# Optimization experiments

Measured on AMD Instinct MI355X. Metric: run time of the kernel, lower is better.

## Reference

```python
import jax, jax.numpy as jnp
import numpy as np

N = 100000
E = 1600000
F_IN = 128
HDIM = 64
HEADS = 8
C1 = HDIM // HEADS  # 8 per-head channels in conv1
NUM_CLASSES = 2
NUM_GRAPHS = 64
NEG_SLOPE = 0.2


def setup_inputs() -> dict:
    key = jax.random.key(0)
    ks = jax.random.split(key, 12)
    x = jax.random.normal(ks[0], (N, F_IN), dtype=jnp.float32)
    edge_index = jax.random.randint(ks[1], (2, E), 0, N, dtype=jnp.int64)
    batch = jnp.sort(jax.random.randint(ks[2], (N,), 0, NUM_GRAPHS, dtype=jnp.int64))
    # conv1 params (Glorot-ish scale)
    W1 = jax.random.normal(ks[3], (F_IN, HEADS * C1), dtype=jnp.float32) * (1.0 / np.sqrt(F_IN))
    att_src1 = jax.random.normal(ks[4], (HEADS, C1), dtype=jnp.float32) * 0.1
    att_dst1 = jax.random.normal(ks[5], (HEADS, C1), dtype=jnp.float32) * 0.1
    b1 = jnp.zeros((HEADS * C1,), dtype=jnp.float32)
    # conv2 params (1 head, no concat)
    W2 = jax.random.normal(ks[6], (HDIM, 1 * NUM_CLASSES), dtype=jnp.float32) * (1.0 / np.sqrt(HDIM))
    att_src2 = jax.random.normal(ks[7], (1, NUM_CLASSES), dtype=jnp.float32) * 0.1
    att_dst2 = jax.random.normal(ks[8], (1, NUM_CLASSES), dtype=jnp.float32) * 0.1
    b2 = jnp.zeros((NUM_CLASSES,), dtype=jnp.float32)
    return {"x": x, "edge_index": edge_index, "batch": batch,
            "W1": W1, "att_src1": att_src1, "att_dst1": att_dst1, "b1": b1,
            "W2": W2, "att_src2": att_src2, "att_dst2": att_dst2, "b2": b2}


def gat_conv(x, src, dst, W, a_src, a_dst, b, heads, ch, concat):
    # PyG GATConv: linear proj -> per-edge attention -> segment softmax over dst -> scatter-add
    n = x.shape[0]
    h = (x @ W).reshape(n, heads, ch)                      # [N,H,C]
    alpha_s = jnp.einsum('nhc,hc->nh', h, a_src)           # [N,H]
    alpha_d = jnp.einsum('nhc,hc->nh', h, a_dst)           # [N,H]
    e = jax.nn.leaky_relu(alpha_s[src] + alpha_d[dst], NEG_SLOPE)  # [E,H]
    m = jax.ops.segment_max(e, dst, num_segments=n)        # stable softmax per dst
    e = jnp.exp(e - m[dst])
    denom = jax.ops.segment_sum(e, dst, num_segments=n) + 1e-16
    alpha = e / denom[dst]                                 # [E,H]
    msg = h[src] * alpha[:, :, None]                       # [E,H,C]
    out = jax.ops.segment_sum(msg, dst, num_segments=n)    # [N,H,C]
    if concat:
        out = out.reshape(n, heads * ch)
    else:
        out = out.mean(axis=1)
    return out + b


def reference(x, edge_index, batch, W1, att_src1, att_dst1, b1, W2, att_src2, att_dst2, b2):
    # PyG GATConv default add_self_loops=True
    loops = jnp.arange(N, dtype=edge_index.dtype)
    src = jnp.concatenate([edge_index[0], loops])
    dst = jnp.concatenate([edge_index[1], loops])
    h = gat_conv(x, src, dst, W1, att_src1, att_dst1, b1, HEADS, C1, concat=True)
    h = jax.nn.relu(h)
    # F.dropout with training=False (eval mode) -> identity
    h = gat_conv(h, src, dst, W2, att_src2, att_dst2, b2, 1, NUM_CLASSES, concat=False)
    # global_mean_pool over batch ids
    sums = jax.ops.segment_sum(h, batch, num_segments=NUM_GRAPHS)
    cnts = jax.ops.segment_sum(jnp.ones((N,), h.dtype), batch, num_segments=NUM_GRAPHS)
    pooled = sums / jnp.maximum(cnts, 1.0)[:, None]        # [G, num_classes]
    return jax.nn.log_softmax(pooled, axis=1)
```

## Files before the change

kernel.cpp:

```cpp
#include <hip/hip_runtime.h>
#include <hip/hip_bf16.h>
#include <hip/hip_fp16.h>
#include <math.h>

#define NN 100000
#define EE 1600000
#define ET 1700000
#define NEG_SLOPE 0.2f
#define XS_STRIDE 136
#define L2E 1.44269504088896f

#define BKB 8
#define BKSZ 256
#define NBUCK 391
#define SLAB 8192
#define PAD 32
#define EPT2 16
#define CHUNK2 (256 * EPT2)
#define NCH2 ((ET + CHUNK2 - 1) / CHUNK2)

typedef _Float16 f16;
typedef f16 f16x8 __attribute__((ext_vector_type(8)));
typedef float f32x4 __attribute__((ext_vector_type(4)));
typedef float f32x2 __attribute__((ext_vector_type(2)));

__device__ __forceinline__ float leaky(float v) {
    return fmaxf(v, NEG_SLOPE * v);
}
__device__ __forceinline__ unsigned char enc_fp8(float v) {
    int pk = __builtin_amdgcn_cvt_pk_fp8_f32(v, 0.f, 0, false);
    return (unsigned char)(pk & 0xff);
}

__device__ __forceinline__ void fold8(float (&dst)[8], const float (&X)[8],
                                      const float (&Y)[8], int sb, int off) {
#pragma unroll
    for (int i = 0; i < 8; ++i) {
        float m = sb ? Y[i] : X[i];
        float o = sb ? X[i] : Y[i];
        dst[i] = m + __shfl_xor(o, off, 64);
    }
}


__global__ __launch_bounds__(256) void convert_w_kernel(
        const float* __restrict__ W1, f16* __restrict__ wt,
        unsigned char* __restrict__ nrec) {
    int i = blockIdx.x * 256 + threadIdx.x;
    if (i < 128 * 64) {
        int n = i >> 7, k = i & 127;
        wt[n * 128 + k] = (f16)W1[k * 64 + n];
    }
    if (blockIdx.x == 0 && threadIdx.x < 8) {
        uint4* dr = (uint4*)(nrec + (size_t)NN * 128);
        dr[threadIdx.x] = make_uint4(0u, 0u, 0xFC00u, 0u);
    }
}

__global__ __launch_bounds__(256) void gemm1_mfma(
        const float* __restrict__ x, const f16* __restrict__ wt,
        const float* __restrict__ att_s, const float* __restrict__ att_d,
        unsigned char* __restrict__ nrec) {
    __shared__ f16 xs[64 * XS_STRIDE];
    const int tid = threadIdx.x;
    const int node0 = blockIdx.x * 64;
    for (int i = tid; i < 64 * 64; i += 256) {
        int r = i >> 6, cp = i & 63;
        int n = node0 + r;
        float2 v = (n < NN) ? ((const float2*)x)[(long)n * 64 + cp]
                            : make_float2(0.f, 0.f);
        xs[r * XS_STRIDE + 2 * cp]     = (f16)v.x;
        xs[r * XS_STRIDE + 2 * cp + 1] = (f16)v.y;
    }
    __syncthreads();
    const int wv = tid >> 6;
    const int lane = tid & 63;
    const int n16 = lane & 15;
    const int quad = lane >> 4;
    f16x8 bf[4][4];
#pragma unroll
    for (int t = 0; t < 4; ++t)
#pragma unroll
        for (int kk = 0; kk < 4; ++kk)
            bf[t][kk] = *(const f16x8*)(wt + ((t * 16 + n16) * 128 + kk * 32 + quad * 8));
    f32x4 acc[4] = {{0,0,0,0},{0,0,0,0},{0,0,0,0},{0,0,0,0}};
#pragma unroll
    for (int kk = 0; kk < 4; ++kk) {
        f16x8 af = *(const f16x8*)(xs + ((wv * 16 + n16) * XS_STRIDE + kk * 32 + quad * 8));
#pragma unroll
        for (int t = 0; t < 4; ++t)
            acc[t] = __builtin_amdgcn_mfma_f32_16x16x32_f16(af, bf[t][kk], acc[t], 0, 0, 0);
    }
    float ats[4], atd[4];
#pragma unroll
    for (int t = 0; t < 4; ++t) {
        ats[t] = att_s[t * 16 + n16];
        atd[t] = att_d[t * 16 + n16];
    }
    const int head = (n16 >> 3);
    const int chpos = n16 & 7;
#pragma unroll
    for (int t = 0; t < 4; ++t)
#pragma unroll
        for (int r = 0; r < 4; ++r) {
            int m = node0 + wv * 16 + quad * 4 + r;
            bool ok = (m < NN);
            if (ok)
                nrec[(size_t)m * 128 + (t * 2 + head) * 16 + chpos] =
                    enc_fp8(acc[t][r]);
            float vs = acc[t][r] * ats[t];
            float vd = acc[t][r] * atd[t];
            vs += __shfl_xor(vs, 1, 64); vd += __shfl_xor(vd, 1, 64);
            vs += __shfl_xor(vs, 2, 64); vd += __shfl_xor(vd, 2, 64);
            vs += __shfl_xor(vs, 4, 64); vd += __shfl_xor(vd, 4, 64);
            if (ok && chpos == 0) {
                unsigned char* nb = nrec + (size_t)m * 128 + (t * 2 + head) * 16;
                *(__half*)(nb + 8)  = __float2half_rn(vs * L2E);
                *(float*)(nb + 12) = vd * L2E;
            }
        }
}

__global__ __launch_bounds__(256) void bucket_fill(
        const int* __restrict__ ei, int* __restrict__ bcur,
        unsigned* __restrict__ gpay) {
    __shared__ int lcnt[NBUCK];
    __shared__ int gbase[NBUCK];
    const int tid = threadIdx.x;
    for (int i = tid; i < NBUCK; i += 256) lcnt[i] = 0;
    __syncthreads();
    const int base = blockIdx.x * CHUNK2 + tid;
    unsigned pay[EPT2];
    int bk[EPT2], pos[EPT2];
#pragma unroll
    for (int k = 0; k < EPT2; ++k) {
        int e = base + k * 256;
        if (e < ET) {
            int s, d;
            if (e < EE) {
                s = __builtin_nontemporal_load(ei + e);
                d = __builtin_nontemporal_load(ei + EE + e);
            } else { s = d = e - EE; }
            int b = d >> BKB;
            bk[k] = b;
            pay[k] = ((unsigned)(d & (BKSZ - 1)) << 17) | (unsigned)s;
            pos[k] = atomicAdd(&lcnt[b], 1);
        } else bk[k] = -1;
    }
    __syncthreads();
    for (int i = tid; i < NBUCK; i += 256)
        gbase[i] = lcnt[i] ? (i * SLAB + atomicAdd(&bcur[i * PAD], lcnt[i])) : 0;
    __syncthreads();
#pragma unroll
    for (int k = 0; k < EPT2; ++k)
        if (bk[k] >= 0) gpay[gbase[bk[k]] + pos[k]] = pay[k];
}

__global__ __launch_bounds__(256) void fine_csr(
        const unsigned* __restrict__ gpay, const int* __restrict__ bcur,
        int* __restrict__ rowptr, int* __restrict__ rowend,
        int* __restrict__ csr_src) {
    __shared__ int cnt[BKSZ];
    __shared__ int ts[256];
    const int b = blockIdx.x;
    const int tid = threadIdx.x;
    const int off = b * SLAB;
    int blen = bcur[b * PAD];
    if (blen > SLAB) blen = SLAB;
    const int d0 = b << BKB;
    cnt[tid] = 0;
    __syncthreads();
    for (int i = tid; i < blen; i += 256)
        atomicAdd(&cnt[gpay[off + i] >> 17], 1);
    __syncthreads();
    int v = cnt[tid];
    int vp = (v + 7) & ~7;
    ts[tid] = vp;
    __syncthreads();
    for (int o = 1; o < 256; o <<= 1) {
        int u = (tid >= o) ? ts[tid - o] : 0;
        __syncthreads();
        ts[tid] += u;
        __syncthreads();
    }
    int excl = ts[tid] - vp;
    if (excl + vp > SLAB) vp = v;
    cnt[tid] = excl;
    int d = d0 + tid;
    if (d < NN) {
        rowptr[d] = off + excl;
        rowend[d] = off + excl + v;
    }
    for (int i = v; i < vp; ++i) csr_src[off + excl + i] = NN;
    __syncthreads();
    for (int i = tid; i < blen; i += 256) {
        unsigned pay = gpay[off + i];
        int pos = atomicAdd(&cnt[pay >> 17], 1);
        csr_src[off + pos] = (int)(pay & 0x1FFFFu);
    }
}

__global__ __launch_bounds__(256) void conv1_fused_kernel(
        const int* __restrict__ rowptr, const int* __restrict__ rowend,
        const int* __restrict__ csr_src, const unsigned char* __restrict__ nrec,
        const float* __restrict__ b1, const float* __restrict__ W2,
        const float* __restrict__ as2, const float* __restrict__ ad2,
        float4* __restrict__ rec) {
    const int tid = threadIdx.x;
    const int wv = tid >> 6;
    const int c = tid & 63;
    const int slot = c >> 3;
    const int hd = c & 7;
    const int sb0 = slot & 1, sb1 = (slot >> 1) & 1, sb2 = (slot >> 2) & 1;
    int n0 = __builtin_amdgcn_readfirstlane((blockIdx.x * 4 + wv) * 4);
    const float adA = *(const float*)(nrec + ((size_t)(n0 + 0) << 7) + (hd << 4) + 12);
    const float adB = *(const float*)(nrec + ((size_t)(n0 + 1) << 7) + (hd << 4) + 12);
    const float adC = *(const float*)(nrec + ((size_t)(n0 + 2) << 7) + (hd << 4) + 12);
    const float adD = *(const float*)(nrec + ((size_t)(n0 + 3) << 7) + (hd << 4) + 12);
    int jA = rowptr[n0 + 0], eA = jA + ((rowend[n0 + 0] - jA + 7) & ~7);
    int jB = rowptr[n0 + 1], eB = jB + ((rowend[n0 + 1] - jB + 7) & ~7);
    int jC = rowptr[n0 + 2], eC = jC + ((rowend[n0 + 2] - jC + 7) & ~7);
    int jD = rowptr[n0 + 3], eD = jD + ((rowend[n0 + 3] - jD + 7) & ~7);
    float accA[8] = {0,0,0,0,0,0,0,0}, accB[8] = {0,0,0,0,0,0,0,0};
    float accC[8] = {0,0,0,0,0,0,0,0}, accD[8] = {0,0,0,0,0,0,0,0};
    float lA = 0.f, lB = 0.f, lC = 0.f, lD = 0.f;

#define STEP(j, e, ad, l, acc)                                               \
    {                                                                        \
        int jj = (j) < (e) - 8 ? (j) : (e) - 8;        \
        int src = csr_src[jj + slot];                                        \
        uint4 v = *(const uint4*)(nrec + (((size_t)src << 7) | (hd << 4)));  \
        unsigned short ush = (unsigned short)v.z;                            \
        float as = __half2float(*(const __half*)&ush);                       \
        float p = exp2f(leaky(as + (ad)));                                   \
        p = ((j) < (e)) ? p : 0.f;                                           \
        f32x2 f01 = __builtin_amdgcn_cvt_pk_f32_fp8((int)v.x, 0);            \
        f32x2 f23 = __builtin_amdgcn_cvt_pk_f32_fp8((int)v.x, 1);            \
        f32x2 f45 = __builtin_amdgcn_cvt_pk_f32_fp8((int)v.y, 0);            \
        f32x2 f67 = __builtin_amdgcn_cvt_pk_f32_fp8((int)v.y, 1);            \
        (l) += p;                                                            \
        acc[0] += p * f01.x; acc[1] += p * f01.y;                            \
        acc[2] += p * f23.x; acc[3] += p * f23.y;                            \
        acc[4] += p * f45.x; acc[5] += p * f45.y;                            \
        acc[6] += p * f67.x; acc[7] += p * f67.y;                            \
        (j) += 8;                                                            \
    }

    while (jA < eA || jB < eB || jC < eC || jD < eD) {
        STEP(jA, eA, adA, lA, accA);
        STEP(jB, eB, adB, lB, accB);
        STEP(jC, eC, adC, lC, accC);
        STEP(jD, eD, adD, lD, accD);
    }
#undef STEP

    float P[8], Q[8];
    fold8(P, accA, accB, sb0, 8);
    fold8(Q, accC, accD, sb0, 8);
    float lP, lQ, lm, lo;
    lm = sb0 ? lB : lA; lo = sb0 ? lA : lB;
    lP = lm + __shfl_xor(lo, 8, 64);
    lm = sb0 ? lD : lC; lo = sb0 ? lC : lD;
    lQ = lm + __shfl_xor(lo, 8, 64);
    float R[8];
    fold8(R, P, Q, sb1, 16);
    lm = sb1 ? lQ : lP; lo = sb1 ? lP : lQ;
    float l = lm + __shfl_xor(lo, 16, 64);
    float S[4];
#pragma unroll
    for (int i = 0; i < 4; ++i) {
        float m = sb2 ? R[i + 4] : R[i];
        float o = sb2 ? R[i] : R[i + 4];
        S[i] = m + __shfl_xor(o, 32, 64);
    }
    l += __shfl_xor(l, 32, 64);
    const int cb = (hd << 3) + sb2 * 4;
    float inv = 1.f / (l + 1e-16f);
    float4 bb = *(const float4*)(b1 + cb);
    float4 w01 = *(const float4*)(W2 + cb * 2);
    float4 w23 = *(const float4*)(W2 + cb * 2 + 4);
    float v0 = fmaxf(S[0] * inv + bb.x, 0.f);
    float v1 = fmaxf(S[1] * inv + bb.y, 0.f);
    float v2 = fmaxf(S[2] * inv + bb.z, 0.f);
    float v3 = fmaxf(S[3] * inv + bb.w, 0.f);
    float r0 = v0 * w01.x + v1 * w01.z + v2 * w23.x + v3 * w23.z;
    float r1 = v0 * w01.y + v1 * w01.w + v2 * w23.y + v3 * w23.w;
    r0 += __shfl_xor(r0, 1, 64);  r1 += __shfl_xor(r1, 1, 64);
    r0 += __shfl_xor(r0, 2, 64);  r1 += __shfl_xor(r1, 2, 64);
    r0 += __shfl_xor(r0, 4, 64);  r1 += __shfl_xor(r1, 4, 64);
    r0 += __shfl_xor(r0, 32, 64); r1 += __shfl_xor(r1, 32, 64);
    if (hd == 0 && sb2 == 0) {
        int n = n0 + sb1 * 2 + sb0;
        rec[n] = make_float4((r0 * as2[0] + r1 * as2[1]) * L2E, r0, r1,
                             (r0 * ad2[0] + r1 * ad2[1]) * L2E);
    }
}

__global__ __launch_bounds__(256) void conv2_pool_kernel(
        const int* __restrict__ rowptr, const int* __restrict__ rowend,
        const int* __restrict__ csr_src, const float4* __restrict__ rec,
        const int* __restrict__ batch,
        float* __restrict__ pooled ) {
    __shared__ float ls[192];
    int tid = threadIdx.x;
    if (tid < 192) ls[tid] = 0.f;
    __syncthreads();
    int n = blockIdx.x * 256 + tid;
    if (n < NN) {
        float adn = rec[n].w;
        int jb = rowptr[n], je = rowend[n];
        float l0 = 0.f, l1 = 0.f, l2 = 0.f, l3 = 0.f;
        float x0 = 0.f, x1 = 0.f, x2 = 0.f, x3 = 0.f;
        float y0 = 0.f, y1 = 0.f, y2 = 0.f, y3 = 0.f;
        int j = jb;
        int i0 = csr_src[j], i1 = csr_src[j + 1];
        int i2 = csr_src[j + 2], i3 = csr_src[j + 3];
        for (; j + 3 < je; ) {
            float4 ra = rec[i0];
            float4 rb = rec[i1];
            float4 rc = rec[i2];
            float4 rd = rec[i3];
            j += 4;
            i0 = csr_src[j] & 0x1FFFF;     i1 = csr_src[j + 1] & 0x1FFFF;
            i2 = csr_src[j + 2] & 0x1FFFF; i3 = csr_src[j + 3] & 0x1FFFF;
            float pa = exp2f(leaky(ra.x + adn));
            float pb = exp2f(leaky(rb.x + adn));
            float pc = exp2f(leaky(rc.x + adn));
            float pd = exp2f(leaky(rd.x + adn));
            l0 += pa; x0 += pa * ra.y; y0 += pa * ra.z;
            l1 += pb; x1 += pb * rb.y; y1 += pb * rb.z;
            l2 += pc; x2 += pc * rc.y; y2 += pc * rc.z;
            l3 += pd; x3 += pd * rd.y; y3 += pd * rd.z;
        }
        for (; j < je; ++j) {
            float4 ra = rec[csr_src[j]];
            float pa = exp2f(leaky(ra.x + adn));
            l0 += pa; x0 += pa * ra.y; y0 += pa * ra.z;
        }
        float l = (l0 + l1) + (l2 + l3);
        float xx = (x0 + x1) + (x2 + x3);
        float yy = (y0 + y1) + (y2 + y3);
        float inv = 1.f / (l + 1e-16f);
        int g = batch[n];
        atomicAdd(&ls[g * 2],     xx * inv);
        atomicAdd(&ls[g * 2 + 1], yy * inv);
        atomicAdd(&ls[128 + g],   1.f);
    }
    __syncthreads();
    if (tid < 192) atomicAdd(&pooled[tid], ls[tid]);
}

__global__ __launch_bounds__(64) void final_kernel(
        const float* __restrict__ pooled, const float* __restrict__ b2,
        float* __restrict__ out) {
    int g = threadIdx.x;
    if (g >= 64) return;
    float c = pooled[128 + g];
    float denom = c > 1.f ? c : 1.f;
    float p0 = pooled[g * 2] / denom + b2[0];
    float p1 = pooled[g * 2 + 1] / denom + b2[1];
    float m = fmaxf(p0, p1);
    float lse = m + logf(expf(p0 - m) + expf(p1 - m));
    out[g * 2] = p0 - lse;
    out[g * 2 + 1] = p1 - lse;
}

extern "C" void kernel_launch(void* const* d_in, const int* in_sizes, int n_in,
                              void* d_out, int out_size, void* d_ws, size_t ws_size,
                              hipStream_t stream) {
    const float* x   = (const float*)d_in[0];
    const int*   ei  = (const int*)d_in[1];
    const int*   bat = (const int*)d_in[2];
    const float* W1  = (const float*)d_in[3];
    const float* as1 = (const float*)d_in[4];
    const float* ad1 = (const float*)d_in[5];
    const float* b1  = (const float*)d_in[6];
    const float* W2  = (const float*)d_in[7];
    const float* as2 = (const float*)d_in[8];
    const float* ad2 = (const float*)d_in[9];
    const float* b2  = (const float*)d_in[10];
    float* out = (float*)d_out;

    float* ws = (float*)d_ws;
    const long off_nrec   = 0;
    const long off_wt     = off_nrec + (long)(NN + 1) * 32;
    const long off_rec    = off_wt + 4096;
    const long off_rowptr = off_rec + (long)NN * 4;
    const long off_rowend = off_rowptr + NN;
    const long off_gpay   = off_rowend + NN;
    const long off_csr    = off_gpay + (long)NBUCK * SLAB;
    const long off_zero   = off_csr + (long)NBUCK * SLAB;
    const long off_bcur   = off_zero;
    const long off_pool   = off_bcur + NBUCK * PAD;
    const long zero_elems = off_pool + 192 - off_zero;

    hipMemsetAsync(ws + off_zero, 0, zero_elems * sizeof(float), stream);

    convert_w_kernel<<<32, 256, 0, stream>>>(W1, (f16*)(ws + off_wt),
                                             (unsigned char*)(ws + off_nrec));
    gemm1_mfma<<<(NN + 63) / 64, 256, 0, stream>>>(
        x, (const f16*)(ws + off_wt), as1, ad1,
        (unsigned char*)(ws + off_nrec));

    bucket_fill<<<NCH2, 256, 0, stream>>>(ei, (int*)(ws + off_bcur),
                                          (unsigned*)(ws + off_gpay));
    fine_csr<<<NBUCK, 256, 0, stream>>>(
        (const unsigned*)(ws + off_gpay), (const int*)(ws + off_bcur),
        (int*)(ws + off_rowptr), (int*)(ws + off_rowend),
        (int*)(ws + off_csr));

    conv1_fused_kernel<<<NN / 16, 256, 0, stream>>>(
        (const int*)(ws + off_rowptr), (const int*)(ws + off_rowend),
        (const int*)(ws + off_csr), (const unsigned char*)(ws + off_nrec),
        b1, W2, as2, ad2, (float4*)(ws + off_rec));

    conv2_pool_kernel<<<(NN + 255) / 256, 256, 0, stream>>>(
        (const int*)(ws + off_rowptr), (const int*)(ws + off_rowend),
        (const int*)(ws + off_csr), (const float4*)(ws + off_rec),
        bat, ws + off_pool);

    final_kernel<<<1, 64, 0, stream>>>(ws + off_pool, b2, out);
}
```

Before: 229.6 us.

## Fuse small kernels, halve bucket size, split conv2 rows over 4 lanes

Folds the weight conversion into bucket_fill and the final log-softmax into conv2_pool_kernel through a last-block-done counter, which removes two kernel launches. Bucket size drops from 256 to 128 nodes, doubling the number of fine_csr blocks. Each conv2 node is now handled by four lanes combined with shuffles, and the x load in gemm1 is widened to float4. Risks include the extra atomic and fence at the end of conv2, and slab overflow with the smaller 4096 slab.

```diff
diff --git a/kernel.cpp b/kernel.cpp
--- a/kernel.cpp
+++ b/kernel.cpp
@@ -10,16 +10,17 @@
 #define XS_STRIDE 136
 #define L2E 1.44269504088896f
 
-#define BKB 8
-#define BKSZ 256
-#define NBUCK 391
-#define SLAB 8192
+#define BKB 7
+#define BKSZ 128
+#define NBUCK 782
+#define SLAB 4096
 #define PAD 32
 #define EPT2 16
 #define CHUNK2 (256 * EPT2)
 #define NCH2 ((ET + CHUNK2 - 1) / CHUNK2)
 
 typedef _Float16 f16;
+typedef f16 f16x4 __attribute__((ext_vector_type(4)));
 typedef f16 f16x8 __attribute__((ext_vector_type(8)));
 typedef float f32x4 __attribute__((ext_vector_type(4)));
 typedef float f32x2 __attribute__((ext_vector_type(2)));
@@ -43,18 +44,49 @@
 }
 
 
-__global__ __launch_bounds__(256) void convert_w_kernel(
-        const float* __restrict__ W1, f16* __restrict__ wt,
-        unsigned char* __restrict__ nrec) {
-    int i = blockIdx.x * 256 + threadIdx.x;
-    if (i < 128 * 64) {
+__global__ __launch_bounds__(256) void bucket_fill(
+        const int* __restrict__ ei, int* __restrict__ bcur,
+        unsigned* __restrict__ gpay, const float* __restrict__ W1,
+        f16* __restrict__ wt, unsigned char* __restrict__ nrec) {
+    const int tid = threadIdx.x;
+    if (blockIdx.x < 32) {
+        int i = blockIdx.x * 256 + tid;
         int n = i >> 7, k = i & 127;
         wt[n * 128 + k] = (f16)W1[k * 64 + n];
     }
-    if (blockIdx.x == 0 && threadIdx.x < 8) {
+    if (blockIdx.x == 32 && tid < 8) {
         uint4* dr = (uint4*)(nrec + (size_t)NN * 128);
-        dr[threadIdx.x] = make_uint4(0u, 0u, 0xFC00u, 0u);
-    }
+        dr[tid] = make_uint4(0u, 0u, 0xFC00u, 0u);
+    }
+    __shared__ int lcnt[NBUCK];
+    __shared__ int gbase[NBUCK];
+    for (int i = tid; i < NBUCK; i += 256) lcnt[i] = 0;
+    __syncthreads();
+    const int base = blockIdx.x * CHUNK2 + tid;
+    unsigned pay[EPT2];
+    int bk[EPT2], pos[EPT2];
+#pragma unroll
+    for (int k = 0; k < EPT2; ++k) {
+        int e = base + k * 256;
+        if (e < ET) {
+            int s, d;
+            if (e < EE) {
+                s = __builtin_nontemporal_load(ei + e);
+                d = __builtin_nontemporal_load(ei + EE + e);
+            } else { s = d = e - EE; }
+            int b = d >> BKB;
+            bk[k] = b;
+            pay[k] = ((unsigned)(d & (BKSZ - 1)) << 17) | (unsigned)s;
+            pos[k] = atomicAdd(&lcnt[b], 1);
+        } else bk[k] = -1;
+    }
+    __syncthreads();
+    for (int i = tid; i < NBUCK; i += 256)
+        gbase[i] = lcnt[i] ? (i * SLAB + atomicAdd(&bcur[i * PAD], lcnt[i])) : 0;
+    __syncthreads();
+#pragma unroll
+    for (int k = 0; k < EPT2; ++k)
+        if (bk[k] >= 0) gpay[gbase[bk[k]] + pos[k]] = pay[k];
 }
 
 __global__ __launch_bounds__(256) void gemm1_mfma(
@@ -64,13 +96,13 @@
     __shared__ f16 xs[64 * XS_STRIDE];
     const int tid = threadIdx.x;
     const int node0 = blockIdx.x * 64;
-    for (int i = tid; i < 64 * 64; i += 256) {
-        int r = i >> 6, cp = i & 63;
+    for (int i = tid; i < 64 * 32; i += 256) {
+        int r = i >> 5, cp = i & 31;
         int n = node0 + r;
-        float2 v = (n < NN) ? ((const float2*)x)[(long)n * 64 + cp]
-                            : make_float2(0.f, 0.f);
-        xs[r * XS_STRIDE + 2 * cp]     = (f16)v.x;
-        xs[r * XS_STRIDE + 2 * cp + 1] = (f16)v.y;
+        float4 v = (n < NN) ? ((const float4*)x)[(long)n * 32 + cp]
+                            : make_float4(0.f, 0.f, 0.f, 0.f);
+        f16x4 h = {(f16)v.x, (f16)v.y, (f16)v.z, (f16)v.w};
+        *(f16x4*)(xs + r * XS_STRIDE + 4 * cp) = h;
     }
     __syncthreads();
     const int wv = tid >> 6;
@@ -121,41 +153,6 @@
         }
 }
 
-__global__ __launch_bounds__(256) void bucket_fill(
-        const int* __restrict__ ei, int* __restrict__ bcur,
-        unsigned* __restrict__ gpay) {
-    __shared__ int lcnt[NBUCK];
-    __shared__ int gbase[NBUCK];
-    const int tid = threadIdx.x;
-    for (int i = tid; i < NBUCK; i += 256) lcnt[i] = 0;
-    __syncthreads();
-    const int base = blockIdx.x * CHUNK2 + tid;
-    unsigned pay[EPT2];
-    int bk[EPT2], pos[EPT2];
-#pragma unroll
-    for (int k = 0; k < EPT2; ++k) {
-        int e = base + k * 256;
-        if (e < ET) {
-            int s, d;
-            if (e < EE) {
-                s = __builtin_nontemporal_load(ei + e);
-                d = __builtin_nontemporal_load(ei + EE + e);
-            } else { s = d = e - EE; }
-            int b = d >> BKB;
-            bk[k] = b;
-            pay[k] = ((unsigned)(d & (BKSZ - 1)) << 17) | (unsigned)s;
-            pos[k] = atomicAdd(&lcnt[b], 1);
-        } else bk[k] = -1;
-    }
-    __syncthreads();
-    for (int i = tid; i < NBUCK; i += 256)
-        gbase[i] = lcnt[i] ? (i * SLAB + atomicAdd(&bcur[i * PAD], lcnt[i])) : 0;
-    __syncthreads();
-#pragma unroll
-    for (int k = 0; k < EPT2; ++k)
-        if (bk[k] >= 0) gpay[gbase[bk[k]] + pos[k]] = pay[k];
-}
-
 __global__ __launch_bounds__(256) void fine_csr(
         const unsigned* __restrict__ gpay, const int* __restrict__ bcur,
         int* __restrict__ rowptr, int* __restrict__ rowend,
@@ -168,12 +165,12 @@
     int blen = bcur[b * PAD];
     if (blen > SLAB) blen = SLAB;
     const int d0 = b << BKB;
-    cnt[tid] = 0;
+    if (tid < BKSZ) cnt[tid] = 0;
     __syncthreads();
     for (int i = tid; i < blen; i += 256)
         atomicAdd(&cnt[gpay[off + i] >> 17], 1);
     __syncthreads();
-    int v = cnt[tid];
+    int v = (tid < BKSZ) ? cnt[tid] : 0;
     int vp = (v + 7) & ~7;
     ts[tid] = vp;
     __syncthreads();
@@ -185,9 +182,9 @@
     }
     int excl = ts[tid] - vp;
     if (excl + vp > SLAB) vp = v;
-    cnt[tid] = excl;
+    if (tid < BKSZ) cnt[tid] = excl;
     int d = d0 + tid;
-    if (d < NN) {
+    if (tid < BKSZ && d < NN) {
         rowptr[d] = off + excl;
         rowend[d] = off + excl + v;
     }
@@ -299,70 +296,55 @@
 __global__ __launch_bounds__(256) void conv2_pool_kernel(
         const int* __restrict__ rowptr, const int* __restrict__ rowend,
         const int* __restrict__ csr_src, const float4* __restrict__ rec,
-        const int* __restrict__ batch,
-        float* __restrict__ pooled ) {
+        const int* __restrict__ batch, float* __restrict__ pooled,
+        int* __restrict__ done, const float* __restrict__ b2,
+        float* __restrict__ out) {
     __shared__ float ls[192];
+    __shared__ int lastBlk;
     int tid = threadIdx.x;
     if (tid < 192) ls[tid] = 0.f;
     __syncthreads();
-    int n = blockIdx.x * 256 + tid;
+    int q = tid & 3;
+    int n = blockIdx.x * 64 + (tid >> 2);
     if (n < NN) {
         float adn = rec[n].w;
         int jb = rowptr[n], je = rowend[n];
-        float l0 = 0.f, l1 = 0.f, l2 = 0.f, l3 = 0.f;
-        float x0 = 0.f, x1 = 0.f, x2 = 0.f, x3 = 0.f;
-        float y0 = 0.f, y1 = 0.f, y2 = 0.f, y3 = 0.f;
-        int j = jb;
-        int i0 = csr_src[j], i1 = csr_src[j + 1];
-        int i2 = csr_src[j + 2], i3 = csr_src[j + 3];
-        for (; j + 3 < je; ) {
-            float4 ra = rec[i0];
-            float4 rb = rec[i1];
-            float4 rc = rec[i2];
-            float4 rd = rec[i3];
-            j += 4;
-            i0 = csr_src[j] & 0x1FFFF;     i1 = csr_src[j + 1] & 0x1FFFF;
-            i2 = csr_src[j + 2] & 0x1FFFF; i3 = csr_src[j + 3] & 0x1FFFF;
-            float pa = exp2f(leaky(ra.x + adn));
-            float pb = exp2f(leaky(rb.x + adn));
-            float pc = exp2f(leaky(rc.x + adn));
-            float pd = exp2f(leaky(rd.x + adn));
-            l0 += pa; x0 += pa * ra.y; y0 += pa * ra.z;
-            l1 += pb; x1 += pb * rb.y; y1 += pb * rb.z;
-            l2 += pc; x2 += pc * rc.y; y2 += pc * rc.z;
-            l3 += pd; x3 += pd * rd.y; y3 += pd * rd.z;
-        }
-        for (; j < je; ++j) {
+        float l = 0.f, xx = 0.f, yy = 0.f;
+        for (int j = jb + q; j < je; j += 4) {
             float4 ra = rec[csr_src[j]];
             float pa = exp2f(leaky(ra.x + adn));
-            l0 += pa; x0 += pa * ra.y; y0 += pa * ra.z;
+            l += pa; xx += pa * ra.y; yy += pa * ra.z;
         }
-        float l = (l0 + l1) + (l2 + l3);
-        float xx = (x0 + x1) + (x2 + x3);
-        float yy = (y0 + y1) + (y2 + y3);
-        float inv = 1.f / (l + 1e-16f);
-        int g = batch[n];
-        atomicAdd(&ls[g * 2],     xx * inv);
-        atomicAdd(&ls[g * 2 + 1], yy * inv);
-        atomicAdd(&ls[128 + g],   1.f);
+        l += __shfl_xor(l, 1, 64); xx += __shfl_xor(xx, 1, 64); yy += __shfl_xor(yy, 1, 64);
+        l += __shfl_xor(l, 2, 64); xx += __shfl_xor(xx, 2, 64); yy += __shfl_xor(yy, 2, 64);
+        if (q == 0) {
+            float inv = 1.f / (l + 1e-16f);
+            int g = batch[n];
+            atomicAdd(&ls[g * 2],     xx * inv);
+            atomicAdd(&ls[g * 2 + 1], yy * inv);
+            atomicAdd(&ls[128 + g],   1.f);
+        }
     }
     __syncthreads();
     if (tid < 192) atomicAdd(&pooled[tid], ls[tid]);
-}
-
-__global__ __launch_bounds__(64) void final_kernel(
-        const float* __restrict__ pooled, const float* __restrict__ b2,
-        float* __restrict__ out) {
-    int g = threadIdx.x;
-    if (g >= 64) return;
-    float c = pooled[128 + g];
-    float denom = c > 1.f ? c : 1.f;
-    float p0 = pooled[g * 2] / denom + b2[0];
-    float p1 = pooled[g * 2 + 1] / denom + b2[1];
-    float m = fmaxf(p0, p1);
-    float lse = m + logf(expf(p0 - m) + expf(p1 - m));
-    out[g * 2] = p0 - lse;
-    out[g * 2 + 1] = p1 - lse;
+    __threadfence();
+    __syncthreads();
+    if (tid == 0) lastBlk = (atomicAdd(done, 1) == (int)gridDim.x - 1);
+    __syncthreads();
+    if (lastBlk && tid < 64) {
+        __threadfence();
+        int g = tid;
+        float cgt = atomicAdd(&pooled[128 + g], 0.f);
+        float s0  = atomicAdd(&pooled[g * 2], 0.f);
+        float s1  = atomicAdd(&pooled[g * 2 + 1], 0.f);
+        float denom = cgt > 1.f ? cgt : 1.f;
+        float p0 = s0 / denom + b2[0];
+        float p1 = s1 / denom + b2[1];
+        float m = fmaxf(p0, p1);
+        float lse = m + logf(expf(p0 - m) + expf(p1 - m));
+        out[g * 2] = p0 - lse;
+        out[g * 2 + 1] = p1 - lse;
+    }
 }
 
 extern "C" void kernel_launch(void* const* d_in, const int* in_sizes, int n_in,
@@ -391,19 +373,20 @@
     const long off_csr    = off_gpay + (long)NBUCK * SLAB;
     const long off_zero   = off_csr + (long)NBUCK * SLAB;
     const long off_bcur   = off_zero;
-    const long off_pool   = off_bcur + NBUCK * PAD;
-    const long zero_elems = off_pool + 192 - off_zero;
+    const long off_pool   = off_bcur + (long)NBUCK * PAD;
+    const long off_done   = off_pool + 192;
+    const long zero_elems = off_done + 1 - off_zero;
 
     hipMemsetAsync(ws + off_zero, 0, zero_elems * sizeof(float), stream);
 
-    convert_w_kernel<<<32, 256, 0, stream>>>(W1, (f16*)(ws + off_wt),
-                                             (unsigned char*)(ws + off_nrec));
+    bucket_fill<<<NCH2, 256, 0, stream>>>(
+        ei, (int*)(ws + off_bcur), (unsigned*)(ws + off_gpay),
+        W1, (f16*)(ws + off_wt), (unsigned char*)(ws + off_nrec));
+
     gemm1_mfma<<<(NN + 63) / 64, 256, 0, stream>>>(
         x, (const f16*)(ws + off_wt), as1, ad1,
         (unsigned char*)(ws + off_nrec));
 
-    bucket_fill<<<NCH2, 256, 0, stream>>>(ei, (int*)(ws + off_bcur),
-                                          (unsigned*)(ws + off_gpay));
     fine_csr<<<NBUCK, 256, 0, stream>>>(
         (const unsigned*)(ws + off_gpay), (const int*)(ws + off_bcur),
         (int*)(ws + off_rowptr), (int*)(ws + off_rowend),
@@ -414,10 +397,8 @@
         (const int*)(ws + off_csr), (const unsigned char*)(ws + off_nrec),
         b1, W2, as2, ad2, (float4*)(ws + off_rec));
 
-    conv2_pool_kernel<<<(NN + 255) / 256, 256, 0, stream>>>(
+    conv2_pool_kernel<<<(NN * 4 + 255) / 256, 256, 0, stream>>>(
         (const int*)(ws + off_rowptr), (const int*)(ws + off_rowend),
         (const int*)(ws + off_csr), (const float4*)(ws + off_rec),
-        bat, ws + off_pool);
-
-    final_kernel<<<1, 64, 0, stream>>>(ws + off_pool, b2, out);
-}
+        bat, ws + off_pool, (int*)(ws + off_done), b2, out);
+}
```

New measurement: 314.1 us. 1.37x slower.
